# Performance work log

Measured on AMD Instinct MI355X. Metric: run time of the kernel, lower is better.

Reference implementation:

```python
import jax, jax.numpy as jnp
import numpy as np

B, Q, K, QSIZE, KSIZE, H, VDIM = 4, 1024, 1024, 256, 256, 32, 256


def setup_inputs() -> dict:
    key = jax.random.key(0)
    ks = jax.random.split(key, 10)
    return {
        "keys": jax.random.normal(ks[0], (B, K, KSIZE), dtype=jnp.float32),
        "queries": jax.random.normal(ks[1], (B, Q, QSIZE), dtype=jnp.float32),
        "values": jax.random.normal(ks[2], (B, K, VDIM), dtype=jnp.float32),
        "valid_lens": jax.random.randint(ks[3], (B,), 1, K + 1, dtype=jnp.int32),
        "W_q": jax.random.normal(ks[4], (QSIZE, H), dtype=jnp.float32) * (QSIZE ** -0.5),
        "b_q": jnp.zeros((H,), dtype=jnp.float32),
        "W_k": jax.random.normal(ks[5], (KSIZE, H), dtype=jnp.float32) * (KSIZE ** -0.5),
        "b_k": jnp.zeros((H,), dtype=jnp.float32),
        "w_v": jax.random.normal(ks[6], (H,), dtype=jnp.float32) * (H ** -0.5),
        "b_v": jnp.zeros((), dtype=jnp.float32),
    }


def reference(keys, queries, values, valid_lens, W_q, b_q, W_k, b_k, w_v, b_v):
    # projected features: (B,K,H) and (B,Q,H)
    fk = keys @ W_k + b_k
    fq = queries @ W_q + b_q
    # broadcast add -> (B,Q,K,H), tanh, then scalar projection -> scores (B,Q,K)
    features = jnp.tanh(fq[:, :, None, :] + fk[:, None, :, :])
    scores = jnp.einsum("bqkh,h->bqk", features, w_v) + b_v
    # masked softmax over key axis: positions >= valid_len get -1e6
    mask = jnp.arange(K)[None, None, :] < valid_lens[:, None, None]
    scores = jnp.where(mask, scores, jnp.float32(-1e6))
    weights = jax.nn.softmax(scores, axis=-1)
    # bmm: (B,Q,K) @ (B,K,V) -> (B,Q,V)
    return jnp.einsum("bqk,bkv->bqv", weights, values)
```

## Files before the change

### kernel.cpp

```cpp
#include <hip/hip_runtime.h>
#include <math.h>


#define NB 4
#define NQ 1024
#define NK 1024
#define DQK 256
#define NH 32
#define NV 256
#define TQ 8
#define BLK 512

__device__ __forceinline__ float fast_rcp(float x) { return __builtin_amdgcn_rcpf(x); }

__global__ __launch_bounds__(256) void proj_kernel(
    const float* __restrict__ queries, const float* __restrict__ keys,
    const float* __restrict__ W_q, const float* __restrict__ b_q,
    const float* __restrict__ W_k, const float* __restrict__ b_k,
    float* __restrict__ eq, float* __restrict__ ek)
{
    const int tid     = blockIdx.x * 256 + threadIdx.x;
    const int row     = tid >> 5;
    const int sub     = tid & 31;
    const int h4      = (sub & 7) * 4;
    const int quarter = sub >> 3;

    const float* src; const float* W; const float* bias; float* dst; int r;
    if (row < NB * NQ) { r = row;           src = queries + (size_t)r * DQK; W = W_q; bias = b_q; dst = eq; }
    else               { r = row - NB * NQ; src = keys    + (size_t)r * DQK; W = W_k; bias = b_k; dst = ek; }

    float a0 = 0.f, a1 = 0.f, a2 = 0.f, a3 = 0.f;
    if (quarter == 0) {
        float4 bv4 = *(const float4*)(bias + h4);
        a0 = bv4.x; a1 = bv4.y; a2 = bv4.z; a3 = bv4.w;
    }
    const int d0 = quarter * 64;
    #pragma unroll 4
    for (int i = d0; i < d0 + 64; i += 4) {
        float4 s  = *(const float4*)(src + i);
        float4 w0 = *(const float4*)(W + (size_t)(i + 0) * NH + h4);
        float4 w1 = *(const float4*)(W + (size_t)(i + 1) * NH + h4);
        float4 w2 = *(const float4*)(W + (size_t)(i + 2) * NH + h4);
        float4 w3 = *(const float4*)(W + (size_t)(i + 3) * NH + h4);
        a0 = fmaf(s.x, w0.x, a0); a1 = fmaf(s.x, w0.y, a1); a2 = fmaf(s.x, w0.z, a2); a3 = fmaf(s.x, w0.w, a3);
        a0 = fmaf(s.y, w1.x, a0); a1 = fmaf(s.y, w1.y, a1); a2 = fmaf(s.y, w1.z, a2); a3 = fmaf(s.y, w1.w, a3);
        a0 = fmaf(s.z, w2.x, a0); a1 = fmaf(s.z, w2.y, a1); a2 = fmaf(s.z, w2.z, a2); a3 = fmaf(s.z, w2.w, a3);
        a0 = fmaf(s.w, w3.x, a0); a1 = fmaf(s.w, w3.y, a1); a2 = fmaf(s.w, w3.z, a2); a3 = fmaf(s.w, w3.w, a3);
    }
    a0 += __shfl_xor(a0, 8, 64);  a1 += __shfl_xor(a1, 8, 64);
    a2 += __shfl_xor(a2, 8, 64);  a3 += __shfl_xor(a3, 8, 64);
    a0 += __shfl_xor(a0, 16, 64); a1 += __shfl_xor(a1, 16, 64);
    a2 += __shfl_xor(a2, 16, 64); a3 += __shfl_xor(a3, 16, 64);
    if (quarter == 0) {
        float4 o;
        o.x = __expf(2.f * a0); o.y = __expf(2.f * a1);
        o.z = __expf(2.f * a2); o.w = __expf(2.f * a3);
        *(float4*)(dst + (size_t)r * NH + h4) = o;
    }
}

__global__ __launch_bounds__(BLK, 4) void attn_kernel(
    const float* __restrict__ eq, const float* __restrict__ ek,
    const float* __restrict__ values, const int* __restrict__ valid_lens,
    const float* __restrict__ w_v, float* __restrict__ out)
{
    __shared__ float s_w[NK][TQ];
    __shared__ float s_part[8][TQ];

    const int t      = threadIdx.x;
    const int b      = blockIdx.x >> 7;
    const int q0     = (blockIdx.x & 127) * TQ;
    const int nvalid = valid_lens[b];
    const int wave   = t >> 6;
    const int lane   = t & 63;
    const int qi     = lane & 7;
    const int kk     = lane >> 3;

    const int kpw  = (nvalid + 7) >> 3;
    const int kbeg = wave * kpw;
    const int kend = min(nvalid, kbeg + kpw);

    float wv[NH];
    #pragma unroll
    for (int h = 0; h < NH; h += 4) {
        float4 w4 = *(const float4*)(w_v + h);
        wv[h] = w4.x; wv[h+1] = w4.y; wv[h+2] = w4.z; wv[h+3] = w4.w;
    }
    float eqr[NH];
    const float* eqp = eq + (size_t)(b * NQ + q0 + qi) * NH;
    #pragma unroll
    for (int h = 0; h < NH; h += 4) {
        float4 e4 = *(const float4*)(eqp + h);
        eqr[h] = e4.x; eqr[h+1] = e4.y; eqr[h+2] = e4.z; eqr[h+3] = e4.w;
    }

    const float* ekbase = ek + (size_t)b * NK * NH;
    float ssum = 0.f;
    for (int k0 = kbeg; k0 < kend; k0 += 8) {
        const int k = k0 + kk;
        if (k < kend) {
            const float* ekp = ekbase + (size_t)k * NH;
            float acc = 0.f;
            #pragma unroll
            for (int h = 0; h < NH; h += 4) {
                float4 e4 = *(const float4*)(ekp + h);
                float u0 = fmaf(eqr[h+0], e4.x, 1.f);
                float u1 = fmaf(eqr[h+1], e4.y, 1.f);
                float u2 = fmaf(eqr[h+2], e4.z, 1.f);
                float u3 = fmaf(eqr[h+3], e4.w, 1.f);
                float d01 = u0 * u1, d23 = u2 * u3;
                float n01 = fmaf(wv[h+0], u1, wv[h+1] * u0);
                float n23 = fmaf(wv[h+2], u3, wv[h+3] * u2);
                float d   = fminf(d01 * d23, 1e38f);
                float n   = fmaf(n01, d23, n23 * d01);
                acc = fmaf(n, fast_rcp(d), acc);
            }
            float e = __expf(-2.f * acc);
            s_w[k][qi] = e;
            ssum += e;
        }
    }

    ssum += __shfl_xor(ssum, 8, 64);
    ssum += __shfl_xor(ssum, 16, 64);
    ssum += __shfl_xor(ssum, 32, 64);
    if (lane < TQ) s_part[wave][lane] = ssum;

    float4 acc0 = {0,0,0,0}, acc1 = {0,0,0,0}, acc2 = {0,0,0,0}, acc3 = {0,0,0,0};
    float4 acc4 = {0,0,0,0}, acc5 = {0,0,0,0}, acc6 = {0,0,0,0}, acc7 = {0,0,0,0};
    const float* vbase = values + (size_t)b * NK * NV + 4 * lane;

#define FMA4(A, W) A.x = fmaf((W), v.x, A.x); A.y = fmaf((W), v.y, A.y); \
                   A.z = fmaf((W), v.z, A.z); A.w = fmaf((W), v.w, A.w);
    #pragma unroll 4
    for (int k = kbeg; k < kend; k++) {
        float4 v  = *(const float4*)(vbase + (size_t)k * NV);
        float4 w0 = *(const float4*)(&s_w[k][0]);
        float4 w1 = *(const float4*)(&s_w[k][4]);
        FMA4(acc0, w0.x); FMA4(acc1, w0.y); FMA4(acc2, w0.z); FMA4(acc3, w0.w);
        FMA4(acc4, w1.x); FMA4(acc5, w1.y); FMA4(acc6, w1.z); FMA4(acc7, w1.w);
    }
#undef FMA4

    __syncthreads();
    float* sred = &s_w[0][0];
    float4* p = (float4*)(sred + (size_t)((wave & 3) * TQ) * 256) + lane;
    if (wave < 4) {
        p[0*64] = acc0; p[1*64] = acc1; p[2*64] = acc2; p[3*64] = acc3;
        p[4*64] = acc4; p[5*64] = acc5; p[6*64] = acc6; p[7*64] = acc7;
    }
    __syncthreads();
    if (wave >= 4) {
        float4 x;
#define ACC4(I, A) x = p[I*64]; x.x += A.x; x.y += A.y; x.z += A.z; x.w += A.w; p[I*64] = x;
        ACC4(0, acc0); ACC4(1, acc1); ACC4(2, acc2); ACC4(3, acc3);
        ACC4(4, acc4); ACC4(5, acc5); ACC4(6, acc6); ACC4(7, acc7);
#undef ACC4
    }
    __syncthreads();

    const int v  = t & 255;
    const int qh = (t >> 8) * 4;
    float* obase = out + (size_t)(b * NQ + q0) * NV + v;
    #pragma unroll
    for (int j = 0; j < 4; j++) {
        const int q = qh + j;
        float tot = 0.f;
        #pragma unroll
        for (int w = 0; w < 8; w++) tot += s_part[w][q];
        float rs = fast_rcp(tot);
        float r = sred[(0*TQ + q) * 256 + v] + sred[(1*TQ + q) * 256 + v]
                + sred[(2*TQ + q) * 256 + v] + sred[(3*TQ + q) * 256 + v];
        obase[(size_t)q * NV] = r * rs;
    }
}

extern "C" void kernel_launch(void* const* d_in, const int* in_sizes, int n_in,
                              void* d_out, int out_size, void* d_ws, size_t ws_size,
                              hipStream_t stream) {
    (void)in_sizes; (void)n_in; (void)out_size; (void)ws_size;
    const float* keys       = (const float*)d_in[0];
    const float* queries    = (const float*)d_in[1];
    const float* values     = (const float*)d_in[2];
    const int*   valid_lens = (const int*)d_in[3];
    const float* W_q        = (const float*)d_in[4];
    const float* b_q        = (const float*)d_in[5];
    const float* W_k        = (const float*)d_in[6];
    const float* b_k        = (const float*)d_in[7];
    const float* w_v        = (const float*)d_in[8];
    float* out = (float*)d_out;

    float* eq = (float*)d_ws;
    float* ek = eq + (size_t)NB * NQ * NH;

    proj_kernel<<<dim3(1024), dim3(256), 0, stream>>>(queries, keys, W_q, b_q, W_k, b_k, eq, ek);
    attn_kernel<<<dim3(NB * (NQ / TQ)), dim3(BLK), 0, stream>>>(eq, ek, values, valid_lens, w_v, out);
}
```

Before: 107.7 us.

## Compute four rows per wave in projection and interleave batches across attention blocks

Result: slower. 113.1 us (+5.0%).

```diff
diff --git a/kernel.cpp b/kernel.cpp
--- a/kernel.cpp
+++ b/kernel.cpp
@@ -19,43 +19,63 @@
     const float* __restrict__ W_k, const float* __restrict__ b_k,
     float* __restrict__ eq, float* __restrict__ ek)
 {
-    const int tid     = blockIdx.x * 256 + threadIdx.x;
-    const int row     = tid >> 5;
-    const int sub     = tid & 31;
-    const int h4      = (sub & 7) * 4;
-    const int quarter = sub >> 3;
-
-    const float* src; const float* W; const float* bias; float* dst; int r;
-    if (row < NB * NQ) { r = row;           src = queries + (size_t)r * DQK; W = W_q; bias = b_q; dst = eq; }
-    else               { r = row - NB * NQ; src = keys    + (size_t)r * DQK; W = W_k; bias = b_k; dst = ek; }
-
-    float a0 = 0.f, a1 = 0.f, a2 = 0.f, a3 = 0.f;
-    if (quarter == 0) {
-        float4 bv4 = *(const float4*)(bias + h4);
-        a0 = bv4.x; a1 = bv4.y; a2 = bv4.z; a3 = bv4.w;
-    }
-    const int d0 = quarter * 64;
-    #pragma unroll 4
-    for (int i = d0; i < d0 + 64; i += 4) {
-        float4 s  = *(const float4*)(src + i);
+    const int tid    = blockIdx.x * 256 + threadIdx.x;
+    const int sub    = tid & 63;
+    const int h4     = (sub & 7) * 4;
+    const int eighth = sub >> 3;
+    const int rg     = tid >> 6;
+
+    const float* srcb; const float* W; const float* bias; float* dst; int r0;
+    if (rg < 1024) { r0 = rg * 4;        srcb = queries; W = W_q; bias = b_q; dst = eq; }
+    else           { r0 = (rg - 1024)*4; srcb = keys;    W = W_k; bias = b_k; dst = ek; }
+    const float* src0 = srcb + (size_t)r0 * DQK;
+    const float* src1 = src0 + DQK;
+    const float* src2 = src1 + DQK;
+    const float* src3 = src2 + DQK;
+
+    float a00=0,a01=0,a02=0,a03=0, a10=0,a11=0,a12=0,a13=0;
+    float a20=0,a21=0,a22=0,a23=0, a30=0,a31=0,a32=0,a33=0;
+
+    const int d0 = eighth * 32;
+    #pragma unroll
+    for (int i = d0; i < d0 + 32; i += 4) {
         float4 w0 = *(const float4*)(W + (size_t)(i + 0) * NH + h4);
         float4 w1 = *(const float4*)(W + (size_t)(i + 1) * NH + h4);
         float4 w2 = *(const float4*)(W + (size_t)(i + 2) * NH + h4);
         float4 w3 = *(const float4*)(W + (size_t)(i + 3) * NH + h4);
-        a0 = fmaf(s.x, w0.x, a0); a1 = fmaf(s.x, w0.y, a1); a2 = fmaf(s.x, w0.z, a2); a3 = fmaf(s.x, w0.w, a3);
-        a0 = fmaf(s.y, w1.x, a0); a1 = fmaf(s.y, w1.y, a1); a2 = fmaf(s.y, w1.z, a2); a3 = fmaf(s.y, w1.w, a3);
-        a0 = fmaf(s.z, w2.x, a0); a1 = fmaf(s.z, w2.y, a1); a2 = fmaf(s.z, w2.z, a2); a3 = fmaf(s.z, w2.w, a3);
-        a0 = fmaf(s.w, w3.x, a0); a1 = fmaf(s.w, w3.y, a1); a2 = fmaf(s.w, w3.z, a2); a3 = fmaf(s.w, w3.w, a3);
-    }
-    a0 += __shfl_xor(a0, 8, 64);  a1 += __shfl_xor(a1, 8, 64);
-    a2 += __shfl_xor(a2, 8, 64);  a3 += __shfl_xor(a3, 8, 64);
-    a0 += __shfl_xor(a0, 16, 64); a1 += __shfl_xor(a1, 16, 64);
-    a2 += __shfl_xor(a2, 16, 64); a3 += __shfl_xor(a3, 16, 64);
-    if (quarter == 0) {
+        float4 s0 = *(const float4*)(src0 + i);
+        float4 s1 = *(const float4*)(src1 + i);
+        float4 s2 = *(const float4*)(src2 + i);
+        float4 s3 = *(const float4*)(src3 + i);
+#define ROW(A0,A1,A2,A3,S) \
+        A0 = fmaf(S.x, w0.x, A0); A1 = fmaf(S.x, w0.y, A1); A2 = fmaf(S.x, w0.z, A2); A3 = fmaf(S.x, w0.w, A3); \
+        A0 = fmaf(S.y, w1.x, A0); A1 = fmaf(S.y, w1.y, A1); A2 = fmaf(S.y, w1.z, A2); A3 = fmaf(S.y, w1.w, A3); \
+        A0 = fmaf(S.z, w2.x, A0); A1 = fmaf(S.z, w2.y, A1); A2 = fmaf(S.z, w2.z, A2); A3 = fmaf(S.z, w2.w, A3); \
+        A0 = fmaf(S.w, w3.x, A0); A1 = fmaf(S.w, w3.y, A1); A2 = fmaf(S.w, w3.z, A2); A3 = fmaf(S.w, w3.w, A3);
+        ROW(a00,a01,a02,a03,s0) ROW(a10,a11,a12,a13,s1)
+        ROW(a20,a21,a22,a23,s2) ROW(a30,a31,a32,a33,s3)
+#undef ROW
+    }
+#define RED(A) A += __shfl_xor(A, 8, 64); A += __shfl_xor(A, 16, 64); A += __shfl_xor(A, 32, 64);
+    RED(a00) RED(a01) RED(a02) RED(a03) RED(a10) RED(a11) RED(a12) RED(a13)
+    RED(a20) RED(a21) RED(a22) RED(a23) RED(a30) RED(a31) RED(a32) RED(a33)
+#undef RED
+    if (eighth == 0) {
+        float4 bv = *(const float4*)(bias + h4);
         float4 o;
-        o.x = __expf(2.f * a0); o.y = __expf(2.f * a1);
-        o.z = __expf(2.f * a2); o.w = __expf(2.f * a3);
-        *(float4*)(dst + (size_t)r * NH + h4) = o;
+        float* d = dst + (size_t)r0 * NH + h4;
+        o.x = __expf(2.f*(a00+bv.x)); o.y = __expf(2.f*(a01+bv.y));
+        o.z = __expf(2.f*(a02+bv.z)); o.w = __expf(2.f*(a03+bv.w));
+        *(float4*)(d) = o;
+        o.x = __expf(2.f*(a10+bv.x)); o.y = __expf(2.f*(a11+bv.y));
+        o.z = __expf(2.f*(a12+bv.z)); o.w = __expf(2.f*(a13+bv.w));
+        *(float4*)(d + NH) = o;
+        o.x = __expf(2.f*(a20+bv.x)); o.y = __expf(2.f*(a21+bv.y));
+        o.z = __expf(2.f*(a22+bv.z)); o.w = __expf(2.f*(a23+bv.w));
+        *(float4*)(d + 2*NH) = o;
+        o.x = __expf(2.f*(a30+bv.x)); o.y = __expf(2.f*(a31+bv.y));
+        o.z = __expf(2.f*(a32+bv.z)); o.w = __expf(2.f*(a33+bv.w));
+        *(float4*)(d + 3*NH) = o;
     }
 }
 
@@ -67,9 +87,11 @@
     __shared__ float s_w[NK][TQ];
     __shared__ float s_part[8][TQ];
 
-    const int t      = threadIdx.x;
-    const int b      = blockIdx.x >> 7;
-    const int q0     = (blockIdx.x & 127) * TQ;
+    const int t  = threadIdx.x;
+    const int x  = blockIdx.x & 7;
+    const int j  = blockIdx.x >> 3;
+    const int b  = x & 3;
+    const int q0 = (j + ((x >> 2) << 6)) * TQ;
     const int nvalid = valid_lens[b];
     const int wave   = t >> 6;
     const int lane   = t & 63;
@@ -151,8 +173,8 @@
     }
     __syncthreads();
     if (wave >= 4) {
-        float4 x;
-#define ACC4(I, A) x = p[I*64]; x.x += A.x; x.y += A.y; x.z += A.z; x.w += A.w; p[I*64] = x;
+        float4 x4;
+#define ACC4(I, A) x4 = p[I*64]; x4.x += A.x; x4.y += A.y; x4.z += A.z; x4.w += A.w; p[I*64] = x4;
         ACC4(0, acc0); ACC4(1, acc1); ACC4(2, acc2); ACC4(3, acc3);
         ACC4(4, acc4); ACC4(5, acc5); ACC4(6, acc6); ACC4(7, acc7);
 #undef ACC4
@@ -163,8 +185,8 @@
     const int qh = (t >> 8) * 4;
     float* obase = out + (size_t)(b * NQ + q0) * NV + v;
     #pragma unroll
-    for (int j = 0; j < 4; j++) {
-        const int q = qh + j;
+    for (int jj = 0; jj < 4; jj++) {
+        const int q = qh + jj;
         float tot = 0.f;
         #pragma unroll
         for (int w = 0; w < 8; w++) tot += s_part[w][q];
@@ -193,6 +215,6 @@
     float* eq = (float*)d_ws;
     float* ek = eq + (size_t)NB * NQ * NH;
 
-    proj_kernel<<<dim3(1024), dim3(256), 0, stream>>>(queries, keys, W_q, b_q, W_k, b_k, eq, ek);
+    proj_kernel<<<dim3(512), dim3(256), 0, stream>>>(queries, keys, W_q, b_q, W_k, b_k, eq, ek);
     attn_kernel<<<dim3(NB * (NQ / TQ)), dim3(BLK), 0, stream>>>(eq, ek, values, valid_lens, w_v, out);
 }
```

## Use bf16 MFMA for weights-times-values with pre-transposed bf16 values

Applied to the files above, without the earlier changes.

Measured after the change: 109.2 us. Within noise of the previous version (+1.4%).

```diff
diff --git a/kernel.cpp b/kernel.cpp
--- a/kernel.cpp
+++ b/kernel.cpp
@@ -10,75 +10,121 @@
 #define NV 256
 #define TQ 8
 #define BLK 512
+#define KSTR 1032
+
+typedef __attribute__((ext_vector_type(8))) short bf16x8;
+typedef __attribute__((ext_vector_type(4))) float f32x4;
 
 __device__ __forceinline__ float fast_rcp(float x) { return __builtin_amdgcn_rcpf(x); }
 
-__global__ __launch_bounds__(256) void proj_kernel(
+__device__ __forceinline__ unsigned int f32_to_bf16_rne(float f) {
+    unsigned int u = __float_as_uint(f);
+    return (u + 0x7fffu + ((u >> 16) & 1u)) >> 16;
+}
+
+__global__ __launch_bounds__(256) void proj_cvt_kernel(
     const float* __restrict__ queries, const float* __restrict__ keys,
     const float* __restrict__ W_q, const float* __restrict__ b_q,
     const float* __restrict__ W_k, const float* __restrict__ b_k,
-    float* __restrict__ eq, float* __restrict__ ek)
+    const float* __restrict__ values,
+    float* __restrict__ eq, float* __restrict__ ek,
+    unsigned short* __restrict__ vt)
 {
-    const int tid     = blockIdx.x * 256 + threadIdx.x;
-    const int row     = tid >> 5;
-    const int sub     = tid & 31;
-    const int h4      = (sub & 7) * 4;
-    const int quarter = sub >> 3;
-
-    const float* src; const float* W; const float* bias; float* dst; int r;
-    if (row < NB * NQ) { r = row;           src = queries + (size_t)r * DQK; W = W_q; bias = b_q; dst = eq; }
-    else               { r = row - NB * NQ; src = keys    + (size_t)r * DQK; W = W_k; bias = b_k; dst = ek; }
-
-    float a0 = 0.f, a1 = 0.f, a2 = 0.f, a3 = 0.f;
-    if (quarter == 0) {
-        float4 bv4 = *(const float4*)(bias + h4);
-        a0 = bv4.x; a1 = bv4.y; a2 = bv4.z; a3 = bv4.w;
-    }
-    const int d0 = quarter * 64;
-    #pragma unroll 4
-    for (int i = d0; i < d0 + 64; i += 4) {
-        float4 s  = *(const float4*)(src + i);
-        float4 w0 = *(const float4*)(W + (size_t)(i + 0) * NH + h4);
-        float4 w1 = *(const float4*)(W + (size_t)(i + 1) * NH + h4);
-        float4 w2 = *(const float4*)(W + (size_t)(i + 2) * NH + h4);
-        float4 w3 = *(const float4*)(W + (size_t)(i + 3) * NH + h4);
-        a0 = fmaf(s.x, w0.x, a0); a1 = fmaf(s.x, w0.y, a1); a2 = fmaf(s.x, w0.z, a2); a3 = fmaf(s.x, w0.w, a3);
-        a0 = fmaf(s.y, w1.x, a0); a1 = fmaf(s.y, w1.y, a1); a2 = fmaf(s.y, w1.z, a2); a3 = fmaf(s.y, w1.w, a3);
-        a0 = fmaf(s.z, w2.x, a0); a1 = fmaf(s.z, w2.y, a1); a2 = fmaf(s.z, w2.z, a2); a3 = fmaf(s.z, w2.w, a3);
-        a0 = fmaf(s.w, w3.x, a0); a1 = fmaf(s.w, w3.y, a1); a2 = fmaf(s.w, w3.z, a2); a3 = fmaf(s.w, w3.w, a3);
-    }
-    a0 += __shfl_xor(a0, 8, 64);  a1 += __shfl_xor(a1, 8, 64);
-    a2 += __shfl_xor(a2, 8, 64);  a3 += __shfl_xor(a3, 8, 64);
-    a0 += __shfl_xor(a0, 16, 64); a1 += __shfl_xor(a1, 16, 64);
-    a2 += __shfl_xor(a2, 16, 64); a3 += __shfl_xor(a3, 16, 64);
-    if (quarter == 0) {
-        float4 o;
-        o.x = __expf(2.f * a0); o.y = __expf(2.f * a1);
-        o.z = __expf(2.f * a2); o.w = __expf(2.f * a3);
-        *(float4*)(dst + (size_t)r * NH + h4) = o;
+    __shared__ float tile[64][65];
+
+    if (blockIdx.x < 1024) {
+        const int tid     = blockIdx.x * 256 + threadIdx.x;
+        const int row     = tid >> 5;
+        const int sub     = tid & 31;
+        const int h4      = (sub & 7) * 4;
+        const int quarter = sub >> 3;
+
+        const float* src; const float* W; const float* bias; float* dst; int r;
+        if (row < NB * NQ) { r = row;           src = queries + (size_t)r * DQK; W = W_q; bias = b_q; dst = eq; }
+        else               { r = row - NB * NQ; src = keys    + (size_t)r * DQK; W = W_k; bias = b_k; dst = ek; }
+
+        float a0 = 0.f, a1 = 0.f, a2 = 0.f, a3 = 0.f;
+        if (quarter == 0) {
+            float4 bv4 = *(const float4*)(bias + h4);
+            a0 = bv4.x; a1 = bv4.y; a2 = bv4.z; a3 = bv4.w;
+        }
+        const int d0 = quarter * 64;
+        #pragma unroll 4
+        for (int i = d0; i < d0 + 64; i += 4) {
+            float4 s  = *(const float4*)(src + i);
+            float4 w0 = *(const float4*)(W + (size_t)(i + 0) * NH + h4);
+            float4 w1 = *(const float4*)(W + (size_t)(i + 1) * NH + h4);
+            float4 w2 = *(const float4*)(W + (size_t)(i + 2) * NH + h4);
+            float4 w3 = *(const float4*)(W + (size_t)(i + 3) * NH + h4);
+            a0 = fmaf(s.x, w0.x, a0); a1 = fmaf(s.x, w0.y, a1); a2 = fmaf(s.x, w0.z, a2); a3 = fmaf(s.x, w0.w, a3);
+            a0 = fmaf(s.y, w1.x, a0); a1 = fmaf(s.y, w1.y, a1); a2 = fmaf(s.y, w1.z, a2); a3 = fmaf(s.y, w1.w, a3);
+            a0 = fmaf(s.z, w2.x, a0); a1 = fmaf(s.z, w2.y, a1); a2 = fmaf(s.z, w2.z, a2); a3 = fmaf(s.z, w2.w, a3);
+            a0 = fmaf(s.w, w3.x, a0); a1 = fmaf(s.w, w3.y, a1); a2 = fmaf(s.w, w3.z, a2); a3 = fmaf(s.w, w3.w, a3);
+        }
+        a0 += __shfl_xor(a0, 8, 64);  a1 += __shfl_xor(a1, 8, 64);
+        a2 += __shfl_xor(a2, 8, 64);  a3 += __shfl_xor(a3, 8, 64);
+        a0 += __shfl_xor(a0, 16, 64); a1 += __shfl_xor(a1, 16, 64);
+        a2 += __shfl_xor(a2, 16, 64); a3 += __shfl_xor(a3, 16, 64);
+        if (quarter == 0) {
+            float4 o;
+            o.x = __expf(2.f * a0); o.y = __expf(2.f * a1);
+            o.z = __expf(2.f * a2); o.w = __expf(2.f * a3);
+            *(float4*)(dst + (size_t)r * NH + h4) = o;
+        }
+    } else {
+        const int bx = blockIdx.x - 1024;
+        const int b  = bx >> 6;
+        const int rr = bx & 63;
+        const int kt = rr & 15;
+        const int vtile = rr >> 4;
+        const int t  = threadIdx.x;
+
+        const float* src = values + ((size_t)b * NK + kt * 64) * NV + vtile * 64;
+        const int kl = t >> 2;
+        const int vc = (t & 3) * 16;
+        float4 x0 = *(const float4*)(src + (size_t)kl * NV + vc);
+        float4 x1 = *(const float4*)(src + (size_t)kl * NV + vc + 4);
+        float4 x2 = *(const float4*)(src + (size_t)kl * NV + vc + 8);
+        float4 x3 = *(const float4*)(src + (size_t)kl * NV + vc + 12);
+        *(float4*)&tile[kl][vc]      = x0;
+        *(float4*)&tile[kl][vc + 4]  = x1;
+        *(float4*)&tile[kl][vc + 8]  = x2;
+        *(float4*)&tile[kl][vc + 12] = x3;
+        __syncthreads();
+
+        const int vl = t >> 2;
+        const int kc = (t & 3) * 16;
+        union { unsigned short u[16]; uint4 q[2]; } o;
+        #pragma unroll
+        for (int j = 0; j < 16; j++)
+            o.u[j] = (unsigned short)f32_to_bf16_rne(tile[kc + j][vl]);
+        unsigned short* dst = vt + ((size_t)(b * NV + vtile * 64 + vl)) * NK + kt * 64 + kc;
+        *(uint4*)dst       = o.q[0];
+        *(uint4*)(dst + 8) = o.q[1];
     }
 }
 
 __global__ __launch_bounds__(BLK, 4) void attn_kernel(
     const float* __restrict__ eq, const float* __restrict__ ek,
-    const float* __restrict__ values, const int* __restrict__ valid_lens,
+    const unsigned short* __restrict__ vt, const int* __restrict__ valid_lens,
     const float* __restrict__ w_v, float* __restrict__ out)
 {
-    __shared__ float s_w[NK][TQ];
+    __shared__ unsigned short s_w16[TQ][KSTR];
     __shared__ float s_part[8][TQ];
 
     const int t      = threadIdx.x;
     const int b      = blockIdx.x >> 7;
     const int q0     = (blockIdx.x & 127) * TQ;
     const int nvalid = valid_lens[b];
+    const int kmax   = (nvalid + 31) & ~31;
     const int wave   = t >> 6;
     const int lane   = t & 63;
     const int qi     = lane & 7;
-    const int kk     = lane >> 3;
-
-    const int kpw  = (nvalid + 7) >> 3;
-    const int kbeg = wave * kpw;
-    const int kend = min(nvalid, kbeg + kpw);
+    const int kp     = lane >> 3;
+
+    const int cw   = ((kmax >> 3) + 15) & ~15;
+    const int kbeg = wave * cw;
+    const int kend = min(kmax, kbeg + cw);
 
     float wv[NH];
     #pragma unroll
@@ -96,29 +142,35 @@
 
     const float* ekbase = ek + (size_t)b * NK * NH;
     float ssum = 0.f;
-    for (int k0 = kbeg; k0 < kend; k0 += 8) {
-        const int k = k0 + kk;
-        if (k < kend) {
-            const float* ekp = ekbase + (size_t)k * NH;
-            float acc = 0.f;
-            #pragma unroll
-            for (int h = 0; h < NH; h += 4) {
-                float4 e4 = *(const float4*)(ekp + h);
-                float u0 = fmaf(eqr[h+0], e4.x, 1.f);
-                float u1 = fmaf(eqr[h+1], e4.y, 1.f);
-                float u2 = fmaf(eqr[h+2], e4.z, 1.f);
-                float u3 = fmaf(eqr[h+3], e4.w, 1.f);
-                float d01 = u0 * u1, d23 = u2 * u3;
-                float n01 = fmaf(wv[h+0], u1, wv[h+1] * u0);
-                float n23 = fmaf(wv[h+2], u3, wv[h+3] * u2);
-                float d   = fminf(d01 * d23, 1e38f);
-                float n   = fmaf(n01, d23, n23 * d01);
-                acc = fmaf(n, fast_rcp(d), acc);
+    for (int k0 = kbeg; k0 < kend; k0 += 16) {
+        const int k = k0 + 2 * kp;
+        float e0 = 0.f, e1 = 0.f;
+        #pragma unroll 2
+        for (int s = 0; s < 2; s++) {
+            if (k + s < nvalid) {
+                const float* ekp = ekbase + (size_t)(k + s) * NH;
+                float acc = 0.f;
+                #pragma unroll
+                for (int h = 0; h < NH; h += 4) {
+                    float4 e4 = *(const float4*)(ekp + h);
+                    float u0 = fmaf(eqr[h+0], e4.x, 1.f);
+                    float u1 = fmaf(eqr[h+1], e4.y, 1.f);
+                    float u2 = fmaf(eqr[h+2], e4.z, 1.f);
+                    float u3 = fmaf(eqr[h+3], e4.w, 1.f);
+                    float d01 = u0 * u1, d23 = u2 * u3;
+                    float n01 = fmaf(wv[h+0], u1, wv[h+1] * u0);
+                    float n23 = fmaf(wv[h+2], u3, wv[h+3] * u2);
+                    float d   = fminf(d01 * d23, 1e38f);
+                    float n   = fmaf(n01, d23, n23 * d01);
+                    acc = fmaf(n, fast_rcp(d), acc);
+                }
+                float e = __expf(-2.f * acc);
+                if (s == 0) e0 = e; else e1 = e;
             }
-            float e = __expf(-2.f * acc);
-            s_w[k][qi] = e;
-            ssum += e;
-        }
+        }
+        unsigned int pk = f32_to_bf16_rne(e0) | (f32_to_bf16_rne(e1) << 16);
+        *(unsigned int*)&s_w16[qi][k] = pk;
+        ssum += e0 + e1;
     }
 
     ssum += __shfl_xor(ssum, 8, 64);
@@ -126,52 +178,36 @@
     ssum += __shfl_xor(ssum, 32, 64);
     if (lane < TQ) s_part[wave][lane] = ssum;
 
-    float4 acc0 = {0,0,0,0}, acc1 = {0,0,0,0}, acc2 = {0,0,0,0}, acc3 = {0,0,0,0};
-    float4 acc4 = {0,0,0,0}, acc5 = {0,0,0,0}, acc6 = {0,0,0,0}, acc7 = {0,0,0,0};
-    const float* vbase = values + (size_t)b * NK * NV + 4 * lane;
-
-#define FMA4(A, W) A.x = fmaf((W), v.x, A.x); A.y = fmaf((W), v.y, A.y); \
-                   A.z = fmaf((W), v.z, A.z); A.w = fmaf((W), v.w, A.w);
-    #pragma unroll 4
-    for (int k = kbeg; k < kend; k++) {
-        float4 v  = *(const float4*)(vbase + (size_t)k * NV);
-        float4 w0 = *(const float4*)(&s_w[k][0]);
-        float4 w1 = *(const float4*)(&s_w[k][4]);
-        FMA4(acc0, w0.x); FMA4(acc1, w0.y); FMA4(acc2, w0.z); FMA4(acc3, w0.w);
-        FMA4(acc4, w1.x); FMA4(acc5, w1.y); FMA4(acc6, w1.z); FMA4(acc7, w1.w);
-    }
-#undef FMA4
-
     __syncthreads();
-    float* sred = &s_w[0][0];
-    float4* p = (float4*)(sred + (size_t)((wave & 3) * TQ) * 256) + lane;
-    if (wave < 4) {
-        p[0*64] = acc0; p[1*64] = acc1; p[2*64] = acc2; p[3*64] = acc3;
-        p[4*64] = acc4; p[5*64] = acc5; p[6*64] = acc6; p[7*64] = acc7;
-    }
-    __syncthreads();
-    if (wave >= 4) {
-        float4 x;
-#define ACC4(I, A) x = p[I*64]; x.x += A.x; x.y += A.y; x.z += A.z; x.w += A.w; p[I*64] = x;
-        ACC4(0, acc0); ACC4(1, acc1); ACC4(2, acc2); ACC4(3, acc3);
-        ACC4(4, acc4); ACC4(5, acc5); ACC4(6, acc6); ACC4(7, acc7);
-#undef ACC4
-    }
-    __syncthreads();
-
-    const int v  = t & 255;
-    const int qh = (t >> 8) * 4;
-    float* obase = out + (size_t)(b * NQ + q0) * NV + v;
-    #pragma unroll
-    for (int j = 0; j < 4; j++) {
-        const int q = qh + j;
-        float tot = 0.f;
+
+    const int n    = lane & 15;
+    const int quad = lane >> 4;
+    f32x4 c0 = {0.f, 0.f, 0.f, 0.f};
+    f32x4 c1 = {0.f, 0.f, 0.f, 0.f};
+    const unsigned short* vt0 = vt + ((size_t)(b * NV + wave * 32 + n)) * NK + quad * 8;
+    const unsigned short* vt1 = vt0 + (size_t)16 * NK;
+    const unsigned short* arow = &s_w16[n & 7][quad * 8];
+
+    for (int k0 = 0; k0 < kmax; k0 += 32) {
+        bf16x8 a = {0,0,0,0,0,0,0,0};
+        if (n < 8) a = *(const bf16x8*)(arow + k0);
+        bf16x8 b0 = *(const bf16x8*)(vt0 + k0);
+        bf16x8 b1 = *(const bf16x8*)(vt1 + k0);
+        c0 = __builtin_amdgcn_mfma_f32_16x16x32_bf16(a, b0, c0, 0, 0, 0);
+        c1 = __builtin_amdgcn_mfma_f32_16x16x32_bf16(a, b1, c1, 0, 0, 0);
+    }
+
+    if (quad < 2) {
         #pragma unroll
-        for (int w = 0; w < 8; w++) tot += s_part[w][q];
-        float rs = fast_rcp(tot);
-        float r = sred[(0*TQ + q) * 256 + v] + sred[(1*TQ + q) * 256 + v]
-                + sred[(2*TQ + q) * 256 + v] + sred[(3*TQ + q) * 256 + v];
-        obase[(size_t)q * NV] = r * rs;
+        for (int r = 0; r < 4; r++) {
+            const int q = quad * 4 + r;
+            float den = s_part[0][q] + s_part[1][q] + s_part[2][q] + s_part[3][q]
+                      + s_part[4][q] + s_part[5][q] + s_part[6][q] + s_part[7][q];
+            float rs = fast_rcp(den);
+            float* ob = out + (size_t)(b * NQ + q0 + q) * NV + wave * 32 + n;
+            ob[0]  = c0[r] * rs;
+            ob[16] = c1[r] * rs;
+        }
     }
 }
 
@@ -192,7 +228,10 @@
 
     float* eq = (float*)d_ws;
     float* ek = eq + (size_t)NB * NQ * NH;
-
-    proj_kernel<<<dim3(1024), dim3(256), 0, stream>>>(queries, keys, W_q, b_q, W_k, b_k, eq, ek);
-    attn_kernel<<<dim3(NB * (NQ / TQ)), dim3(BLK), 0, stream>>>(eq, ek, values, valid_lens, w_v, out);
-}
+    unsigned short* vt = (unsigned short*)(ek + (size_t)NB * NK * NH);
+
+    proj_cvt_kernel<<<dim3(1280), dim3(256), 0, stream>>>(
+        queries, keys, W_q, b_q, W_k, b_k, values, eq, ek, vt);
+    attn_kernel<<<dim3(NB * (NQ / TQ)), dim3(BLK), 0, stream>>>(
+        eq, ek, vt, valid_lens, w_v, out);
+}
```
